# Performance work log

Measured on AMD Instinct MI355X. Metric: run time of the kernel, lower is better.

The kernel has to match this reference:

```python
import jax, jax.numpy as jnp
import numpy as np

B, LQ, LKV, D, H, LOOKBACK = 4, 4096, 512, 512, 8, 8
DH = D // H
SCALE = DH ** -0.5


def setup_inputs() -> dict:
    key = jax.random.key(0)
    ks = jax.random.split(key, 12)
    q = jax.random.normal(ks[0], (B, LQ, D), dtype=jnp.float32)
    kv_src = jax.random.normal(ks[1], (B, LKV, D), dtype=jnp.float32)
    seg_id = jnp.sort(jax.random.randint(ks[2], (B, LQ), 0, LKV), axis=-1)
    kv_mask = jnp.zeros((B, LKV), dtype=bool)
    q_pad_mask = jnp.zeros((B, LQ), dtype=bool)
    s = D ** -0.5
    Wq = jax.random.normal(ks[3], (D, D), jnp.float32) * s
    bq = jnp.zeros((D,), jnp.float32)
    Wk = jax.random.normal(ks[4], (D, D), jnp.float32) * s
    bk = jnp.zeros((D,), jnp.float32)
    Wv = jax.random.normal(ks[5], (D, D), jnp.float32) * s
    bv = jnp.zeros((D,), jnp.float32)
    Wo = jax.random.normal(ks[6], (D, D), jnp.float32) * s
    bo = jnp.zeros((D,), jnp.float32)
    return {"q": q, "kv_src": kv_src, "seg_id": seg_id, "kv_mask": kv_mask,
            "q_pad_mask": q_pad_mask, "Wq": Wq, "bq": bq, "Wk": Wk, "bk": bk,
            "Wv": Wv, "bv": bv, "Wo": Wo, "bo": bo}


def _split_heads(x):
    b, l, _ = x.shape
    return x.reshape(b, l, H, DH).transpose(0, 2, 1, 3)  # (B,H,L,Dh)


def reference(q, kv_src, seg_id, kv_mask, q_pad_mask, Wq, bq, Wk, bk, Wv, bv, Wo, bo):
    qh = _split_heads(q @ Wq + bq)        # (B,H,Lq,Dh)
    kh = _split_heads(kv_src @ Wk + bk)   # (B,H,Lkv,Dh)
    vh = _split_heads(kv_src @ Wv + bv)   # (B,H,Lkv,Dh)

    offsets = jnp.arange(LOOKBACK + 1)
    gather = jnp.clip(seg_id[:, :, None] - offsets, 0, LKV - 1)  # (B,Lq,Kw)

    # per-batch windowed gather of K/V: (B,H,Lq,Kw,Dh)
    k_sel = jax.vmap(lambda kb, gb: kb[:, gb])(kh, gather)
    v_sel = jax.vmap(lambda vb, gb: vb[:, gb])(vh, gather)

    scores = jnp.einsum('bhld,bhlkd->bhlk', qh, k_sel) * SCALE
    mask_sel = jax.vmap(lambda m, g: m[g])(kv_mask, gather)  # (B,Lq,Kw)
    scores = jnp.where(mask_sel[:, None], jnp.finfo(scores.dtype).min, scores)
    probs = jax.nn.softmax(scores, axis=-1)

    out = jnp.einsum('bhlk,bhlkd->bhld', probs, v_sel)
    out = out.transpose(0, 2, 1, 3).reshape(q.shape[0], q.shape[1], D)
    out = out @ Wo + bo
    out = jnp.where(q_pad_mask[:, :, None], 0.0, out)
    return out
```

## Files before the change

### kernel.cpp

```cpp
#include <hip/hip_runtime.h>
#include <hip/hip_bf16.h>
#include <float.h>

typedef unsigned short u16;
typedef __attribute__((ext_vector_type(8))) short short8;
typedef __attribute__((ext_vector_type(4))) float f32x4;

#define NB       4
#define LQ       4096
#define LKV      512
#define DMODEL   512
#define NH       8
#define DH       64
#define KW       9
#define SCALE    0.125f

#define BM 64
#define BN 128
#define BK 32

__device__ inline float bf2f(u16 v) { return __uint_as_float(((unsigned)v) << 16); }
__device__ inline u16 f2bf(float f) {
    unsigned u = __float_as_uint(f);
    return (u16)((u + 0x7fffu + ((u >> 16) & 1u)) >> 16);
}
__device__ inline void gload16(const u16* g, u16* l) {
    __builtin_amdgcn_global_load_lds((const __attribute__((address_space(1))) void*)g,
                                     (__attribute__((address_space(3))) void*)l, 16, 0, 0);
}
__device__ inline short8 cvt8(const float4 v0, const float4 v1) {
    short8 s;
    s[0] = (short)f2bf(v0.x); s[1] = (short)f2bf(v0.y);
    s[2] = (short)f2bf(v0.z); s[3] = (short)f2bf(v0.w);
    s[4] = (short)f2bf(v1.x); s[5] = (short)f2bf(v1.y);
    s[6] = (short)f2bf(v1.z); s[7] = (short)f2bf(v1.w);
    return s;
}

__global__ __launch_bounds__(256) void transpose4_kernel(
    const float* __restrict__ Wq, const float* __restrict__ Wk,
    const float* __restrict__ Wv, const float* __restrict__ Wo,
    u16* __restrict__ Wqt, u16* __restrict__ Wkvt, u16* __restrict__ Wot)
{
    __shared__ float tile[32][33];
    const int z = blockIdx.z;
    const float* src = (z == 0) ? Wq : (z == 1) ? Wk : (z == 2) ? Wv : Wo;
    u16* dst = (z == 0) ? Wqt : (z == 3) ? Wot : Wkvt;
    const int roff = (z == 2) ? DMODEL : 0;

    const int tx = threadIdx.x & 31, ty = threadIdx.x >> 5;
    const int x0 = blockIdx.x * 32, y0 = blockIdx.y * 32;
    #pragma unroll
    for (int i = 0; i < 4; ++i)
        tile[ty + i * 8][tx] = src[(y0 + ty + i * 8) * DMODEL + x0 + tx];
    __syncthreads();
    #pragma unroll
    for (int i = 0; i < 4; ++i)
        dst[(long long)(roff + x0 + ty + i * 8) * DMODEL + y0 + tx] = f2bf(tile[tx][ty + i * 8]);
}

template<int A_F32, int OUT_F32>
__global__ __launch_bounds__(256, 4) void gemm64_kernel(
    const void* __restrict__ Ain, const u16* __restrict__ Bt,
    const float* __restrict__ bias0, const float* __restrict__ bias1, int nsplit,
    void* __restrict__ Cout, int M, int N, int K,
    const unsigned char* __restrict__ row_mask)
{
    __shared__ u16 As[BM * BK];
    __shared__ u16 Bs[BN * BK];

    const int tid = threadIdx.x;
    const int w = tid >> 6, l = tid & 63;
    const int wr = w >> 1, wc = w & 1;
    const int brow = blockIdx.y * BM, bcol = blockIdx.x * BN;

    const int rsub = l >> 2;
    const int csrc = (l & 3) ^ (rsub & 3);
    const u16*   gA  = (const u16*)Ain   + (long long)(brow + w * 16 + rsub) * K + csrc * 8;
    const float* gAf = (const float*)Ain + (long long)(brow + w * 16 + rsub) * K + csrc * 8;
    const u16* gB0 = Bt + (long long)(bcol + w * 32 + rsub) * K + csrc * 8;
    const u16* gB1 = gB0 + (long long)16 * K;
    u16* lA  = As + (w * 16) * BK;
    u16* lB0 = Bs + (w * 32) * BK;
    u16* lB1 = Bs + (w * 32 + 16) * BK;

    const int hi = l >> 4, lr = l & 15;
    const int cs = ((hi ^ (lr & 3)) * 8);

    f32x4 acc[2][4] = {};

    for (int k0 = 0; k0 < K; k0 += BK) {
        if (A_F32) {
            const float4 v0 = *(const float4*)(gAf + k0);
            const float4 v1 = *(const float4*)(gAf + k0 + 4);
            *(short8*)(lA + l * 8) = cvt8(v0, v1);
        } else {
            gload16(gA + k0, lA);
        }
        gload16(gB0 + k0, lB0);
        gload16(gB1 + k0, lB1);
        __syncthreads();

        short8 a[2], b[4];
        #pragma unroll
        for (int m = 0; m < 2; ++m)
            a[m] = *(const short8*)&As[(wr * 32 + m * 16 + lr) * BK + cs];
        #pragma unroll
        for (int n = 0; n < 4; ++n)
            b[n] = *(const short8*)&Bs[(wc * 64 + n * 16 + lr) * BK + cs];
        #pragma unroll
        for (int m = 0; m < 2; ++m)
            #pragma unroll
            for (int n = 0; n < 4; ++n)
                acc[m][n] = __builtin_amdgcn_mfma_f32_16x16x32_bf16(a[m], b[n], acc[m][n], 0, 0, 0);
        __syncthreads();
    }

    #pragma unroll
    for (int m = 0; m < 2; ++m) {
        #pragma unroll
        for (int n = 0; n < 4; ++n) {
            const int col = bcol + wc * 64 + n * 16 + lr;
            const float bv = (col < nsplit) ? bias0[col] : bias1[col - nsplit];
            #pragma unroll
            for (int r = 0; r < 4; ++r) {
                const int row = brow + wr * 32 + m * 16 + hi * 4 + r;
                const float v = acc[m][n][r] + bv;
                if (OUT_F32) {
                    ((float*)Cout)[(long long)row * N + col] =
                        (row_mask != nullptr && row_mask[row]) ? 0.0f : v;
                } else {
                    ((u16*)Cout)[(long long)row * N + col] = f2bf(v);
                }
            }
        }
    }
}

__global__ __launch_bounds__(256, 4) void qproj_attn_kernel(
    const float* __restrict__ Aq, const u16* __restrict__ Bt,
    const float* __restrict__ bias, const u16* __restrict__ khv,
    const int* __restrict__ seg_id, const unsigned char* __restrict__ kv_mask,
    u16* __restrict__ atb)
{
    __shared__ u16 As[BM * BK];
    __shared__ u16 Bs[BN * BK];
    __shared__ u16 qt[BM * BN];

    const int tid = threadIdx.x;
    const int w = tid >> 6, l = tid & 63;
    const int wr = w >> 1, wc = w & 1;
    const int brow = blockIdx.y * BM, bcol = blockIdx.x * BN;
    const int K = DMODEL;

    const int rsub = l >> 2;
    const int csrc = (l & 3) ^ (rsub & 3);
    const float* gAf = Aq + (long long)(brow + w * 16 + rsub) * K + csrc * 8;
    const u16* gB0 = Bt + (long long)(bcol + w * 32 + rsub) * K + csrc * 8;
    const u16* gB1 = gB0 + (long long)16 * K;
    u16* lA  = As + (w * 16) * BK;
    u16* lB0 = Bs + (w * 32) * BK;
    u16* lB1 = Bs + (w * 32 + 16) * BK;

    const int hi = l >> 4, lr = l & 15;
    const int cs = ((hi ^ (lr & 3)) * 8);

    f32x4 acc[2][4] = {};

    for (int k0 = 0; k0 < K; k0 += BK) {
        const float4 v0 = *(const float4*)(gAf + k0);
        const float4 v1 = *(const float4*)(gAf + k0 + 4);
        *(short8*)(lA + l * 8) = cvt8(v0, v1);
        gload16(gB0 + k0, lB0);
        gload16(gB1 + k0, lB1);
        __syncthreads();

        short8 a[2], b[4];
        #pragma unroll
        for (int m = 0; m < 2; ++m)
            a[m] = *(const short8*)&As[(wr * 32 + m * 16 + lr) * BK + cs];
        #pragma unroll
        for (int n = 0; n < 4; ++n)
            b[n] = *(const short8*)&Bs[(wc * 64 + n * 16 + lr) * BK + cs];
        #pragma unroll
        for (int m = 0; m < 2; ++m)
            #pragma unroll
            for (int n = 0; n < 4; ++n)
                acc[m][n] = __builtin_amdgcn_mfma_f32_16x16x32_bf16(a[m], b[n], acc[m][n], 0, 0, 0);
        __syncthreads();
    }

    #pragma unroll
    for (int m = 0; m < 2; ++m) {
        #pragma unroll
        for (int n = 0; n < 4; ++n) {
            const int col = wc * 64 + n * 16 + lr;
            const float bv = bias[bcol + col];
            const int g = col >> 3;
            #pragma unroll
            for (int r = 0; r < 4; ++r) {
                const int row = wr * 32 + m * 16 + hi * 4 + r;
                qt[row * BN + ((g ^ (row & 7)) << 3) + (col & 7)] =
                    f2bf(acc[m][n][r] + bv);
            }
        }
    }
    __syncthreads();

    const int dchunk = tid & 7;
    #pragma unroll
    for (int p = 0; p < 4; ++p) {
        const int it = p * 32 + (tid >> 3);
        const int row = it >> 1;
        const int h2  = it & 1;
        const long long bl = brow + row;
        const int b = (int)(bl >> 12);
        const int head = (bcol >> 6) + h2;
        const int seg = seg_id[bl];
        const unsigned char* km = kv_mask + b * LKV;
        const u16* kvb = khv + (long long)b * LKV * 1024;

        const int g = h2 * 8 + dchunk;
        const short8 q8 = *(const short8*)&qt[row * BN + ((g ^ (row & 7)) << 3)];
        float qf[8];
        #pragma unroll
        for (int e = 0; e < 8; ++e) qf[e] = bf2f((u16)q8[e]);

        int idxs[KW];
        float sc[KW];
        #pragma unroll
        for (int j = 0; j < KW; ++j) {
            int idx = seg - j;
            idx = idx < 0 ? 0 : (idx > LKV - 1 ? LKV - 1 : idx);
            idxs[j] = idx;
            const short8 k8 = *(const short8*)&kvb[(long long)idx * 1024 + head * DH + dchunk * 8];
            float d = 0.0f;
            #pragma unroll
            for (int e = 0; e < 8; ++e)
                d = fmaf(qf[e], bf2f((u16)k8[e]), d);
            d += __shfl_xor(d, 1);
            d += __shfl_xor(d, 2);
            d += __shfl_xor(d, 4);
            float s = d * SCALE;
            if (km[idx]) s = -FLT_MAX;
            sc[j] = s;
        }

        float mx = sc[0];
        #pragma unroll
        for (int j = 1; j < KW; ++j) mx = fmaxf(mx, sc[j]);
        float den = 0.0f;
        #pragma unroll
        for (int j = 0; j < KW; ++j) { sc[j] = __expf(sc[j] - mx); den += sc[j]; }
        const float inv = 1.0f / den;

        float o[8];
        #pragma unroll
        for (int e = 0; e < 8; ++e) o[e] = 0.0f;
        #pragma unroll
        for (int j = 0; j < KW; ++j) {
            const short8 v8 = *(const short8*)&kvb[(long long)idxs[j] * 1024 + DMODEL + head * DH + dchunk * 8];
            const float pj = sc[j];
            #pragma unroll
            for (int e = 0; e < 8; ++e)
                o[e] = fmaf(pj, bf2f((u16)v8[e]), o[e]);
        }

        short8 ov;
        #pragma unroll
        for (int e = 0; e < 8; ++e) ov[e] = (short)f2bf(o[e] * inv);
        *(short8*)&atb[bl * DMODEL + head * DH + dchunk * 8] = ov;
    }
}

extern "C" void kernel_launch(void* const* d_in, const int* in_sizes, int n_in,
                              void* d_out, int out_size, void* d_ws, size_t ws_size,
                              hipStream_t stream) {
    const float*         q          = (const float*)d_in[0];
    const float*         kv_src     = (const float*)d_in[1];
    const int*           seg_id     = (const int*)d_in[2];
    const unsigned char* kv_mask    = (const unsigned char*)d_in[3];
    const unsigned char* q_pad_mask = (const unsigned char*)d_in[4];
    const float*         Wq         = (const float*)d_in[5];
    const float*         bq         = (const float*)d_in[6];
    const float*         Wk         = (const float*)d_in[7];
    const float*         bk         = (const float*)d_in[8];
    const float*         Wv         = (const float*)d_in[9];
    const float*         bv         = (const float*)d_in[10];
    const float*         Wo         = (const float*)d_in[11];
    const float*         bo         = (const float*)d_in[12];
    float* out = (float*)d_out;

    const long long MQ  = (long long)NB * LQ;
    const long long MKV = (long long)NB * LKV;

    char* wsb = (char*)d_ws;
    u16* Wqt  = (u16*)wsb;  wsb += DMODEL * DMODEL * 2;
    u16* Wkvt = (u16*)wsb;  wsb += 2 * DMODEL * DMODEL * 2;
    u16* Wot  = (u16*)wsb;  wsb += DMODEL * DMODEL * 2;
    u16* khv  = (u16*)wsb;  wsb += MKV * 2 * DMODEL * 2;
    u16* atb  = (u16*)wsb;  wsb += MQ  * DMODEL * 2;

    dim3 blk(256);

    transpose4_kernel<<<dim3(DMODEL / 32, DMODEL / 32, 4), blk, 0, stream>>>(
        Wq, Wk, Wv, Wo, Wqt, Wkvt, Wot);

    gemm64_kernel<1, 0><<<dim3(2 * DMODEL / BN, MKV / BM), blk, 0, stream>>>(
        kv_src, Wkvt, bk, bv, DMODEL, khv, (int)MKV, 2 * DMODEL, DMODEL, nullptr);

    qproj_attn_kernel<<<dim3(DMODEL / BN, MQ / BM), blk, 0, stream>>>(
        q, Wqt, bq, khv, seg_id, kv_mask, atb);

    gemm64_kernel<0, 1><<<dim3(DMODEL / BN, MQ / BM), blk, 0, stream>>>(
        atb, Wot, bo, bo, DMODEL, out, (int)MQ, DMODEL, DMODEL, q_pad_mask);
}
```

Measured before the change: 87.96 us.

## Add XCD-aware block swizzle, register prefetch of fp32 A, and shared-memory aliasing

Flattens the launch grids to 1D and remaps block IDs so consecutive tiles sharing the same rows land on the same XCD, aiming for better L2 reuse across the chiplets. It also prefetches the next fp32 A tile into registers after the barrier so the global load latency overlaps with the MFMA work. In the fused Q-projection/attention kernel, the As/Bs staging buffers now alias the qt buffer to cut LDS use. Launch bounds are raised from 4 to 6 waves-per-SIMD target to allow higher occupancy, at the cost of more register pressure and possible spills.

```diff
diff --git a/kernel.cpp b/kernel.cpp
--- a/kernel.cpp
+++ b/kernel.cpp
@@ -35,6 +35,10 @@
     s[4] = (short)f2bf(v1.x); s[5] = (short)f2bf(v1.y);
     s[6] = (short)f2bf(v1.z); s[7] = (short)f2bf(v1.w);
     return s;
+}
+__device__ inline int xcd_swz(int id, int nwg) {
+    const int cpx = nwg >> 3;
+    return (id & 7) * cpx + (id >> 3);
 }
 
 __global__ __launch_bounds__(256) void transpose4_kernel(
@@ -60,10 +64,10 @@
 }
 
 template<int A_F32, int OUT_F32>
-__global__ __launch_bounds__(256, 4) void gemm64_kernel(
+__global__ __launch_bounds__(256, 6) void gemm64_kernel(
     const void* __restrict__ Ain, const u16* __restrict__ Bt,
     const float* __restrict__ bias0, const float* __restrict__ bias1, int nsplit,
-    void* __restrict__ Cout, int M, int N, int K,
+    void* __restrict__ Cout, int M, int N, int K, int cshift,
     const unsigned char* __restrict__ row_mask)
 {
     __shared__ u16 As[BM * BK];
@@ -72,7 +76,11 @@
     const int tid = threadIdx.x;
     const int w = tid >> 6, l = tid & 63;
     const int wr = w >> 1, wc = w & 1;
-    const int brow = blockIdx.y * BM, bcol = blockIdx.x * BN;
+
+    const int wg = xcd_swz((int)blockIdx.x, (int)gridDim.x);
+    const int bx = wg & ((1 << cshift) - 1);
+    const int by = wg >> cshift;
+    const int brow = by * BM, bcol = bx * BN;
 
     const int rsub = l >> 2;
     const int csrc = (l & 3) ^ (rsub & 3);
@@ -89,10 +97,11 @@
 
     f32x4 acc[2][4] = {};
 
+    float4 v0, v1;
+    if (A_F32) { v0 = *(const float4*)(gAf); v1 = *(const float4*)(gAf + 4); }
+
     for (int k0 = 0; k0 < K; k0 += BK) {
         if (A_F32) {
-            const float4 v0 = *(const float4*)(gAf + k0);
-            const float4 v1 = *(const float4*)(gAf + k0 + 4);
             *(short8*)(lA + l * 8) = cvt8(v0, v1);
         } else {
             gload16(gA + k0, lA);
@@ -100,6 +109,11 @@
         gload16(gB0 + k0, lB0);
         gload16(gB1 + k0, lB1);
         __syncthreads();
+
+        if (A_F32 && k0 + BK < K) {
+            v0 = *(const float4*)(gAf + k0 + BK);
+            v1 = *(const float4*)(gAf + k0 + BK + 4);
+        }
 
         short8 a[2], b[4];
         #pragma unroll
@@ -137,20 +151,25 @@
     }
 }
 
-__global__ __launch_bounds__(256, 4) void qproj_attn_kernel(
+__global__ __launch_bounds__(256, 6) void qproj_attn_kernel(
     const float* __restrict__ Aq, const u16* __restrict__ Bt,
     const float* __restrict__ bias, const u16* __restrict__ khv,
     const int* __restrict__ seg_id, const unsigned char* __restrict__ kv_mask,
     u16* __restrict__ atb)
 {
-    __shared__ u16 As[BM * BK];
-    __shared__ u16 Bs[BN * BK];
-    __shared__ u16 qt[BM * BN];
+    __shared__ u16 smem[BM * BN];
+    u16* As = smem;
+    u16* Bs = smem + BM * BK;
+    u16* qt = smem;
 
     const int tid = threadIdx.x;
     const int w = tid >> 6, l = tid & 63;
     const int wr = w >> 1, wc = w & 1;
-    const int brow = blockIdx.y * BM, bcol = blockIdx.x * BN;
+
+    const int wg = xcd_swz((int)blockIdx.x, (int)gridDim.x);
+    const int bx = wg & 3;
+    const int by = wg >> 2;
+    const int brow = by * BM, bcol = bx * BN;
     const int K = DMODEL;
 
     const int rsub = l >> 2;
@@ -167,13 +186,19 @@
 
     f32x4 acc[2][4] = {};
 
+    float4 v0 = *(const float4*)(gAf);
+    float4 v1 = *(const float4*)(gAf + 4);
+
     for (int k0 = 0; k0 < K; k0 += BK) {
-        const float4 v0 = *(const float4*)(gAf + k0);
-        const float4 v1 = *(const float4*)(gAf + k0 + 4);
         *(short8*)(lA + l * 8) = cvt8(v0, v1);
         gload16(gB0 + k0, lB0);
         gload16(gB1 + k0, lB1);
         __syncthreads();
+
+        if (k0 + BK < K) {
+            v0 = *(const float4*)(gAf + k0 + BK);
+            v1 = *(const float4*)(gAf + k0 + BK + 4);
+        }
 
         short8 a[2], b[4];
         #pragma unroll
@@ -306,12 +331,12 @@
     transpose4_kernel<<<dim3(DMODEL / 32, DMODEL / 32, 4), blk, 0, stream>>>(
         Wq, Wk, Wv, Wo, Wqt, Wkvt, Wot);
 
-    gemm64_kernel<1, 0><<<dim3(2 * DMODEL / BN, MKV / BM), blk, 0, stream>>>(
-        kv_src, Wkvt, bk, bv, DMODEL, khv, (int)MKV, 2 * DMODEL, DMODEL, nullptr);
-
-    qproj_attn_kernel<<<dim3(DMODEL / BN, MQ / BM), blk, 0, stream>>>(
+    gemm64_kernel<1, 0><<<dim3((unsigned)((2 * DMODEL / BN) * (MKV / BM))), blk, 0, stream>>>(
+        kv_src, Wkvt, bk, bv, DMODEL, khv, (int)MKV, 2 * DMODEL, DMODEL, 3, nullptr);
+
+    qproj_attn_kernel<<<dim3((unsigned)((DMODEL / BN) * (MQ / BM))), blk, 0, stream>>>(
         q, Wqt, bq, khv, seg_id, kv_mask, atb);
 
-    gemm64_kernel<0, 1><<<dim3(DMODEL / BN, MQ / BM), blk, 0, stream>>>(
-        atb, Wot, bo, bo, DMODEL, out, (int)MQ, DMODEL, DMODEL, q_pad_mask);
-}
+    gemm64_kernel<0, 1><<<dim3((unsigned)((DMODEL / BN) * (MQ / BM))), blk, 0, stream>>>(
+        atb, Wot, bo, bo, DMODEL, out, (int)MQ, DMODEL, DMODEL, 2, q_pad_mask);
+}
```

Result: faster. 83.09 us (-5.5%).
